# Performance work log

Hardware: AMD Instinct MI355X
Metric: run time of the kernel (lower is better)

## Reference

```python
import jax, jax.numpy as jnp
import numpy as np
from itertools import combinations

UNSPOOL = np.array([h + b for h in combinations(range(0, 4), 2) for b in combinations(range(4, 9), 3)])  # (60,5)
EMB = 64

def _lrelu(v):
    return jax.nn.leaky_relu(v, 0.01)

def _unspool(x):
    # x: (M,18) int -> (1,M,60,5) ranks, suits
    x = x[None]
    ranks, suits = x[:, :, ::2], x[:, :, 1::2]
    hr, hs = ranks[:, :, :4], suits[:, :, :4]
    br, bs = ranks[:, :, 4:], suits[:, :, 4:]
    hi, bi = jnp.argsort(hs, -1), jnp.argsort(bs, -1)
    hr = jnp.take_along_axis(hr, hi, -1); hs = jnp.take_along_axis(hs, hi, -1)
    br = jnp.take_along_axis(br, bi, -1); bs = jnp.take_along_axis(bs, bi, -1)
    hi2, bi2 = jnp.argsort(hr, -1), jnp.argsort(br, -1)
    r = jnp.concatenate([jnp.take_along_axis(hr, hi2, -1), jnp.take_along_axis(br, bi2, -1)], -1)
    s = jnp.concatenate([jnp.take_along_axis(hs, hi2, -1), jnp.take_along_axis(bs, bi2, -1)], -1)
    return r[:, :, UNSPOOL], s[:, :, UNSPOOL]

def setup_inputs() -> dict:
    key = jax.random.key(0)
    ks = jax.random.split(key, 24)
    M, nA = 2048, 9
    ranks = jax.random.randint(ks[0], (M, 9), 1, 14)
    suits = jax.random.randint(ks[1], (M, 9), 1, 5)
    x = jnp.zeros((M, 18), jnp.int64 if jax.config.jax_enable_x64 else jnp.int32)
    x = x.at[:, ::2].set(ranks).at[:, 1::2].set(suits)
    def lin(k, i, o):
        kw, kb = jax.random.split(k)
        s = 1.0 / np.sqrt(i)
        return (jax.random.uniform(kw, (i, o), jnp.float32, -s, s),
                jax.random.uniform(kb, (o,), jnp.float32, -s, s))
    emb = jax.random.normal(ks[2], (53, EMB), jnp.float32)
    emb = emb.at[0].set(0.0)  # padding_idx=0
    hW1, hb1 = lin(ks[3], 128, 512); hW2, hb2 = lin(ks[4], 512, 128)
    bW1, bb1 = lin(ks[5], 192, 512); bW2, bb2 = lin(ks[6], 512, 128)
    oW1, ob1 = lin(ks[7], 15360, 512); oW2, ob2 = lin(ks[8], 512, 256); oW3, ob3 = lin(ks[9], 256, 127)
    sW, sb = lin(ks[10], 127, nA)
    return dict(x=x, emb=emb, hW1=hW1, hb1=hb1, hW2=hW2, hb2=hb2,
                bW1=bW1, bb1=bb1, bW2=bW2, bb2=bb2,
                oW1=oW1, ob1=ob1, oW2=oW2, ob2=ob2, oW3=oW3, ob3=ob3,
                sW=sW, sb=sb)

def reference(x, emb, hW1, hb1, hW2, hb2, bW1, bb1, bW2, bb2,
              oW1, ob1, oW2, ob2, oW3, ob3, sW, sb):
    M = x.shape[0]
    sr, ss = _unspool(x)                      # (1,M,60,5)
    cards = (sr - 1) * ss                     # 0..48, 0 is padding
    e = emb[cards]                            # (1,M,60,5,64)
    hero = e[..., :2, :].reshape(1, M, 60, 2 * EMB)    # (1,M,60,128)
    board = e[..., 2:, :].reshape(1, M, 60, 3 * EMB)   # (1,M,60,192)
    hero = _lrelu(_lrelu(hero @ hW1 + hb1) @ hW2 + hb2)
    board = _lrelu(_lrelu(board @ bW1 + bb1) @ bW2 + bb2)
    raw = jnp.concatenate([hero, board], -1).reshape(1, M, 60 * 256)  # (1,M,15360)
    r = _lrelu(raw @ oW1 + ob1)
    r = _lrelu(r @ oW2 + ob2)
    r = _lrelu(r @ oW3 + ob3)
    return r.reshape(M, -1) @ sW + sb         # (M,nA)
```

## Files before the change

kernel.cpp:

```cpp
#include <hip/hip_runtime.h>

typedef _Float16 f16;
typedef __attribute__((ext_vector_type(8))) _Float16 f16x8;
typedef __attribute__((ext_vector_type(4))) _Float16 f16x4;
typedef __attribute__((ext_vector_type(4))) float f32x4;
typedef __attribute__((ext_vector_type(16))) float f32x16;

__device__ inline float lrelu(float v){ return v > 0.f ? v : 0.01f*v; }
__device__ inline f16x8 lrelu8(f16x8 v){
    f16x8 z = {};
    f16x8 mx = __builtin_elementwise_max(v, z);
    f16x8 mn = __builtin_elementwise_min(v, z);
    return mx + mn * (f16)0.01f;
}

__device__ __forceinline__ void gload16(const void* gp, void* lp) {
    __builtin_amdgcn_global_load_lds(
        (const __attribute__((address_space(1))) unsigned int*)gp,
        (__attribute__((address_space(3))) unsigned int*)lp,
        16, 0, 0);
}

#define M_ROWS 2048

#define P1_T    0
#define P1_HW2  265
#define P1_BW2  393
#define P1_OW2  521
#define P1_OW3  777
#define P1_CARD 841
#define P1_END  845

__device__ void d_transpose512(const float* __restrict__ in, f16* __restrict__ out,
                               int K, int Nin, int Nout, int b, int tid) {
    int idx = b * 512 + tid;
    if (idx >= Nout * K) return;
    int n = idx / K, k = idx - n * K;
    float v = (n < Nin) ? in[(size_t)k * Nin + n] : 0.f;
    out[idx] = (f16)v;
}

__global__ __launch_bounds__(512) void prep1(const int* __restrict__ x,
                                             const float* __restrict__ emb,
                                             const float* __restrict__ hW1,
                                             const float* __restrict__ hb1,
                                             const float* __restrict__ hW2,
                                             const float* __restrict__ bW1,
                                             const float* __restrict__ bb1,
                                             const float* __restrict__ bW2,
                                             const float* __restrict__ oW2,
                                             const float* __restrict__ oW3,
                                             f16* __restrict__ T,
                                             f16* __restrict__ hW2t,
                                             f16* __restrict__ bW2t,
                                             f16* __restrict__ oW2t,
                                             f16* __restrict__ oW3t,
                                             int* __restrict__ cid) {
    const int bid = blockIdx.x, tid = threadIdx.x;
    if (bid < P1_HW2) {
        int b = bid;
        int slot = b / 53, card = b - slot * 53;
        const float* W = (slot < 2) ? (hW1 + slot * 64 * 512) : (bW1 + (slot - 2) * 64 * 512);
        const float* e = emb + card * 64;
        float acc = (slot == 1) ? hb1[tid] : ((slot == 4) ? bb1[tid] : 0.f);
        #pragma unroll 8
        for (int k = 0; k < 64; ++k) acc += e[k] * W[k * 512 + tid];
        T[(size_t)b * 512 + tid] = (f16)acc;
    } else if (bid < P1_BW2) {
        d_transpose512(hW2, hW2t, 512, 128, 128, bid - P1_HW2, tid);
    } else if (bid < P1_OW2) {
        d_transpose512(bW2, bW2t, 512, 128, 128, bid - P1_BW2, tid);
    } else if (bid < P1_OW3) {
        d_transpose512(oW2, oW2t, 512, 256, 256, bid - P1_OW2, tid);
    } else if (bid < P1_CARD) {
        d_transpose512(oW3, oW3t, 256, 127, 128, bid - P1_OW3, tid);
    } else {
        int m = (bid - P1_CARD) * 512 + tid;
        if (m >= M_ROWS) return;
        int kh[4], kb[5];
        #pragma unroll
        for (int i = 0; i < 4; ++i) { int r = x[m*18 + 2*i], s = x[m*18 + 2*i + 1]; kh[i] = r*8 + s; }
        #pragma unroll
        for (int i = 0; i < 5; ++i) { int r = x[m*18 + 8 + 2*i], s = x[m*18 + 9 + 2*i]; kb[i] = r*8 + s; }
        #pragma unroll
        for (int i = 1; i < 4; ++i) { int v = kh[i], j = i-1; while (j >= 0 && kh[j] > v) { kh[j+1]=kh[j]; --j; } kh[j+1]=v; }
        #pragma unroll
        for (int i = 1; i < 5; ++i) { int v = kb[i], j = i-1; while (j >= 0 && kb[j] > v) { kb[j+1]=kb[j]; --j; } kb[j+1]=v; }
        #pragma unroll
        for (int i = 0; i < 4; ++i) { int r = kh[i] >> 3, s = kh[i] & 7; cid[m*9 + i] = (r - 1) * s; }
        #pragma unroll
        for (int i = 0; i < 5; ++i) { int r = kb[i] >> 3, s = kb[i] & 7; cid[m*9 + 4 + i] = (r - 1) * s; }
    }
}

#define MG_L2   256
#define MG_END  768

__global__ __launch_bounds__(512, 4) void mega(const int* __restrict__ cid,
                                               const f16* __restrict__ T,
                                               const f16* __restrict__ hW2t,
                                               const f16* __restrict__ bW2t,
                                               const float* __restrict__ hb2,
                                               const float* __restrict__ bb2,
                                               const float* __restrict__ oW1,
                                               f16* __restrict__ X,
                                               f16* __restrict__ Wct) {
    __shared__ __align__(16) char smem[51200];
    const int bid = blockIdx.x, tid = threadIdx.x;

    if (bid < MG_L2) {
        float (*tile)[65] = (float(*)[65])smem;
        int kb = bid & 31, nb = bid >> 5;
        int nl = tid & 63;
        for (int kl = tid >> 6; kl < 64; kl += 8) {
            int col = kb * 64 + kl;
            int p = col >> 7, r = col & 127;
            int n = nb * 64 + nl;
            float s = 0.f;
            if (p < 6) {
                #pragma unroll
                for (int j = 0; j < 10; ++j) s += oW1[(size_t)((p * 10 + j) * 256 + r) * 512 + n];
            } else {
                int t = p - 6;
                #pragma unroll
                for (int i = 0; i < 6; ++i) s += oW1[(size_t)((i * 10 + t) * 256 + 128 + r) * 512 + n];
            }
            tile[kl][nl] = s;
        }
        __syncthreads();
        for (int nl2 = tid >> 6; nl2 < 64; nl2 += 8) {
            int kl2 = tid & 63;
            Wct[(size_t)(nb * 64 + nl2) * 2048 + kb * 64 + kl2] = (f16)tile[kl2][nl2];
        }
        return;
    }

    f16 (*As)[64*64]  = (f16(*)[64*64])smem;
    f16 (*Bs)[128*64] = (f16(*)[128*64])(smem + 16384);
    const int lbid = bid - MG_L2;
    const bool hero = lbid < 192;
    const int row0 = hero ? lbid * 64 : (lbid - 192) * 64;
    const f16* Bt = hero ? hW2t : bW2t;
    const float* bias = hero ? hb2 : bb2;
    const int lane = tid & 63, wave = tid >> 6;
    const int rw = wave & 1, cw = wave >> 1;
    const int l31 = lane & 31, lh = lane >> 5;

    const int br = tid >> 3, bchunk = tid & 7;
    const int grow = row0 + br;
    const f16 *t0, *t1, *t2;
    if (hero) {
        const int HP0[6] = {0,0,0,1,1,2}, HP1[6] = {1,2,3,2,3,3};
        int m = grow / 6, p = grow - m * 6;
        t0 = T + (size_t)(0*53 + cid[m*9 + HP0[p]]) * 512;
        t1 = T + (size_t)(1*53 + cid[m*9 + HP1[p]]) * 512;
        t2 = T;
    } else {
        const int BT0[10] = {4,4,4,4,4,4,5,5,5,6};
        const int BT1[10] = {5,5,5,6,6,7,6,6,7,7};
        const int BT2[10] = {6,7,8,7,8,8,7,8,8,8};
        int m = grow / 10, t = grow - m * 10;
        t0 = T + (size_t)(2*53 + cid[m*9 + BT0[t]]) * 512;
        t1 = T + (size_t)(3*53 + cid[m*9 + BT1[t]]) * 512;
        t2 = T + (size_t)(4*53 + cid[m*9 + BT2[t]]) * 512;
    }

    auto stageB = [&](int buf, int k0) {
        #pragma unroll
        for (int i = 0; i < 2; ++i) {
            int c = tid + i * 512;
            int r = c >> 3, cc = c & 7;
            gload16(Bt + (size_t)r * 512 + k0 + ((cc ^ (r & 7)) << 3), (void*)&Bs[buf][c * 8]);
        }
    };
    auto buildA = [&](int buf, int k0) {
        f16x8 a = *(const f16x8*)(t0 + k0 + bchunk * 8);
        f16x8 b = *(const f16x8*)(t1 + k0 + bchunk * 8);
        f16x8 c = *(const f16x8*)(t2 + k0 + bchunk * 8);
        *(f16x8*)&As[buf][br * 64 + ((bchunk ^ (br & 7)) << 3)] = lrelu8(a + b + c);
    };

    f32x16 acc = {};
    stageB(0, 0); buildA(0, 0);
    __syncthreads();
    for (int t = 0; t < 8; ++t) {
        int cur = t & 1;
        if (t < 7) { stageB(cur ^ 1, (t + 1) * 64); buildA(cur ^ 1, (t + 1) * 64); }
        #pragma unroll
        for (int ks4 = 0; ks4 < 4; ++ks4) {
            int chunk = ks4 * 2 + lh;
            int ar = rw * 32 + l31, bcol = cw * 32 + l31;
            f16x8 a = *(const f16x8*)&As[cur][ar * 64 + ((chunk ^ (ar & 7)) << 3)];
            f16x8 b = *(const f16x8*)&Bs[cur][bcol * 64 + ((chunk ^ (bcol & 7)) << 3)];
            acc = __builtin_amdgcn_mfma_f32_32x32x16_f16(a, b, acc, 0, 0, 0);
        }
        __syncthreads();
    }
    #pragma unroll
    for (int q = 0; q < 16; ++q) {
        int row = row0 + rw * 32 + (q & 3) + 8 * (q >> 2) + 4 * lh;
        int col = cw * 32 + l31;
        float v = lrelu(acc[q] + bias[col]);
        size_t off;
        if (hero) { int m = row / 6,  p = row - m*6;  off = (size_t)m*2048 + p*128 + col; }
        else      { int m = row / 10, p = row - m*10; off = (size_t)m*2048 + 768 + p*128 + col; }
        X[off] = (f16)v;
    }
}

__global__ __launch_bounds__(512, 4) void combine(const f16* __restrict__ X,
                                                  const f16* __restrict__ Wct,
                                                  float* __restrict__ R1p) {
    __shared__ __align__(16) f16 As[2][64 * 64];
    __shared__ __align__(16) f16 Bs[2][128 * 64];
    const int bid = blockIdx.x;
    const int xcd = bid & 7, slot = bid >> 3;
    const int rp = xcd * 4 + (slot & 3);
    const int rest = slot >> 2;
    const int cp = rest & 3, ks = rest >> 2;
    const int row0 = rp * 64, col0 = cp * 128, k0b = ks * 512;
    const int tid = threadIdx.x, lane = tid & 63, wave = tid >> 6;
    const int rw = wave & 1, cw = wave >> 1;
    const int l31 = lane & 31, lh = lane >> 5;

    auto stage = [&](int buf, int k0) {
        { int r = tid >> 3, cc = tid & 7;
          gload16(X + (size_t)(row0 + r) * 2048 + k0 + ((cc ^ (r & 7)) << 3), (void*)&As[buf][tid * 8]); }
        #pragma unroll
        for (int i = 0; i < 2; ++i) {
            int c = tid + i * 512;
            int r = c >> 3, cc = c & 7;
            gload16(Wct + (size_t)(col0 + r) * 2048 + k0 + ((cc ^ (r & 7)) << 3), (void*)&Bs[buf][c * 8]);
        }
    };

    f32x16 acc = {};
    stage(0, k0b);
    __syncthreads();
    for (int t = 0; t < 8; ++t) {
        int cur = t & 1;
        if (t < 7) stage(cur ^ 1, k0b + (t + 1) * 64);
        #pragma unroll
        for (int ks4 = 0; ks4 < 4; ++ks4) {
            int chunk = ks4 * 2 + lh;
            int ar = rw * 32 + l31, bcol = cw * 32 + l31;
            f16x8 a = *(const f16x8*)&As[cur][ar * 64 + ((chunk ^ (ar & 7)) << 3)];
            f16x8 b = *(const f16x8*)&Bs[cur][bcol * 64 + ((chunk ^ (bcol & 7)) << 3)];
            acc = __builtin_amdgcn_mfma_f32_32x32x16_f16(a, b, acc, 0, 0, 0);
        }
        __syncthreads();
    }
    float* dst = R1p + (size_t)ks * 2048 * 512;
    #pragma unroll
    for (int q = 0; q < 16; ++q) {
        int row = row0 + rw * 32 + (q & 3) + 8 * (q >> 2) + 4 * lh;
        int col = col0 + cw * 32 + l31;
        dst[(size_t)row * 512 + col] = acc[q];
    }
}

__global__ __launch_bounds__(512, 2) void tail2(const float* __restrict__ R1p,
                                                const float* __restrict__ ob1,
                                                const f16* __restrict__ oW2t,
                                                const float* __restrict__ ob2,
                                                const f16* __restrict__ oW3t,
                                                const float* __restrict__ ob3,
                                                const float* __restrict__ sW,
                                                const float* __restrict__ sb,
                                                float* __restrict__ out) {
    __shared__ __align__(16) f16 A1s[16 * 512];
    __shared__ __align__(16) f16 Bs[2][256 * 64];
    __shared__ __align__(16) f16 R2s[16 * 256];
    __shared__ float R3s[16][132];
    __shared__ float sWs[127 * 9];
    __shared__ float sbs[9];
    const int row0 = blockIdx.x * 8;
    const int tid = threadIdx.x, lane = tid & 63, wave = tid >> 6;
    const int lr = lane & 15;

    auto stageB2 = [&](int buf, int t) {
        #pragma unroll
        for (int i = 0; i < 4; ++i) {
            int c = tid + i * 512;
            int r = c >> 3, cc = c & 7;
            gload16(oW2t + (size_t)r * 512 + t * 64 + ((cc ^ (r & 7)) << 3), (void*)&Bs[buf][c * 8]);
        }
    };
    stageB2(0, 0);

    #pragma unroll
    for (int i = 0; i < 2; ++i) {
        int g = tid + i * 512;
        int row = g >> 7, c4 = (g & 127) << 2;
        f32x4 v = *(const f32x4*)(ob1 + c4);
        #pragma unroll
        for (int s = 0; s < 4; ++s)
            v += *(const f32x4*)(R1p + (size_t)s * 2048 * 512 + (size_t)(row0 + row) * 512 + c4);
        f16x4 p;
        #pragma unroll
        for (int q = 0; q < 4; ++q) p[q] = (f16)lrelu(v[q]);
        int chunk = c4 >> 3, half = (c4 >> 2) & 1;
        *(f16x4*)&A1s[row * 512 + ((chunk ^ (row & 7)) << 3) + half * 4] = p;
    }
    {
        f16x8 z = {};
        int row = 8 + (tid >> 6), chunk = tid & 63;
        *(f16x8*)&A1s[row * 512 + chunk * 8] = z;
    }
    for (int i = tid; i < 127 * 9; i += 512) sWs[i] = sW[i];
    if (tid < 9) sbs[tid] = sb[tid];
    __syncthreads();

    f32x4 acc2[2] = {};
    for (int t = 0; t < 8; ++t) {
        int cur = t & 1;
        if (t < 7) stageB2(cur ^ 1, t + 1);
        #pragma unroll
        for (int kk2 = 0; kk2 < 2; ++kk2) {
            int g  = kk2 * 4 + (lane >> 4);
            int gg = t * 8 + g;
            f16x8 a = *(const f16x8*)&A1s[lr * 512 + ((gg ^ (lr & 7)) << 3)];
            int eo = (g ^ (lr & 7)) << 3;
            #pragma unroll
            for (int j = 0; j < 2; ++j) {
                f16x8 b = *(const f16x8*)&Bs[cur][(wave * 32 + j * 16 + lr) * 64 + eo];
                acc2[j] = __builtin_amdgcn_mfma_f32_16x16x32_f16(a, b, acc2[j], 0, 0, 0);
            }
        }
        __syncthreads();
    }
    #pragma unroll
    for (int j = 0; j < 2; ++j)
    #pragma unroll
    for (int q = 0; q < 4; ++q) {
        int row = (lane >> 4) * 4 + q;
        int col = wave * 32 + j * 16 + lr;
        f16 v = (f16)lrelu(acc2[j][q] + ob2[col]);
        int chunk = col >> 3, w = col & 7;
        R2s[row * 256 + ((chunk ^ (row & 7)) << 3) + w] = v;
    }
    auto stageB3 = [&](int buf, int t) {
        #pragma unroll
        for (int i = 0; i < 2; ++i) {
            int c = tid + i * 512;
            if (c < 1024) {
                int r = c >> 3, cc = c & 7;
                gload16(oW3t + (size_t)r * 256 + t * 64 + ((cc ^ (r & 7)) << 3), (void*)&Bs[buf][c * 8]);
            }
        }
    };
    stageB3(0, 0);
    __syncthreads();

    f32x4 acc3 = {};
    for (int t = 0; t < 4; ++t) {
        int cur = t & 1;
        if (t < 3) stageB3(cur ^ 1, t + 1);
        #pragma unroll
        for (int kk2 = 0; kk2 < 2; ++kk2) {
            int g  = kk2 * 4 + (lane >> 4);
            int gg = t * 8 + g;
            f16x8 a = *(const f16x8*)&R2s[lr * 256 + ((gg ^ (lr & 7)) << 3)];
            int eo = (g ^ (lr & 7)) << 3;
            f16x8 b = *(const f16x8*)&Bs[cur][(wave * 16 + lr) * 64 + eo];
            acc3 = __builtin_amdgcn_mfma_f32_16x16x32_f16(a, b, acc3, 0, 0, 0);
        }
        __syncthreads();
    }
    #pragma unroll
    for (int q = 0; q < 4; ++q) {
        int row = (lane >> 4) * 4 + q;
        int col = wave * 16 + lr;
        R3s[row][col] = lrelu(acc3[q] + ((col < 127) ? ob3[col] : 0.f));
    }
    __syncthreads();

    if (tid < 8 * 9) {
        int row = tid / 9, a = tid - row * 9;
        float s = sbs[a];
        #pragma unroll 4
        for (int n = 0; n < 127; ++n) s += R3s[row][n] * sWs[n * 9 + a];
        out[(size_t)(row0 + row) * 9 + a] = s;
    }
}

extern "C" void kernel_launch(void* const* d_in, const int* in_sizes, int n_in,
                              void* d_out, int out_size, void* d_ws, size_t ws_size,
                              hipStream_t stream) {
    const int*   x    = (const int*)  d_in[0];
    const float* emb  = (const float*)d_in[1];
    const float* hW1  = (const float*)d_in[2];
    const float* hb1  = (const float*)d_in[3];
    const float* hW2  = (const float*)d_in[4];
    const float* hb2  = (const float*)d_in[5];
    const float* bW1  = (const float*)d_in[6];
    const float* bb1  = (const float*)d_in[7];
    const float* bW2  = (const float*)d_in[8];
    const float* bb2  = (const float*)d_in[9];
    const float* oW1  = (const float*)d_in[10];
    const float* ob1  = (const float*)d_in[11];
    const float* oW2  = (const float*)d_in[12];
    const float* ob2  = (const float*)d_in[13];
    const float* oW3  = (const float*)d_in[14];
    const float* ob3  = (const float*)d_in[15];
    const float* sW   = (const float*)d_in[16];
    const float* sb   = (const float*)d_in[17];

    char* ws = (char*)d_ws;
    constexpr size_t OFF_T    = 0;
    constexpr size_t OFF_HW2T = 271360;
    constexpr size_t OFF_BW2T = 402432;
    constexpr size_t OFF_OW2T = 533504;
    constexpr size_t OFF_OW3T = 795648;
    constexpr size_t OFF_WCT  = 861184;
    constexpr size_t OFF_CID  = 2958336;
    constexpr size_t OFF_X    = 3032064;
    constexpr size_t OFF_R1P  = 11420672;

    f16*   T    = (f16*)(ws + OFF_T);
    f16*   hW2t = (f16*)(ws + OFF_HW2T);
    f16*   bW2t = (f16*)(ws + OFF_BW2T);
    f16*   oW2t = (f16*)(ws + OFF_OW2T);
    f16*   oW3t = (f16*)(ws + OFF_OW3T);
    f16*   Wct  = (f16*)(ws + OFF_WCT);
    int*   cid  = (int*)(ws + OFF_CID);
    f16*   X    = (f16*)(ws + OFF_X);
    float* R1p  = (float*)(ws + OFF_R1P);

    prep1<<<P1_END, 512, 0, stream>>>(x, emb, hW1, hb1, hW2, bW1, bb1, bW2,
                                      oW2, oW3, T, hW2t, bW2t, oW2t, oW3t, cid);
    mega<<<MG_END, 512, 0, stream>>>(cid, T, hW2t, bW2t, hb2, bb2, oW1, X, Wct);
    combine<<<512, 512, 0, stream>>>(X, Wct, R1p);
    tail2<<<256, 512, 0, stream>>>(R1p, ob1, oW2t, ob2, oW3t, ob3, sW, sb, (float*)d_out);
}
```

Before: 53.68 us.

## Move oW1 reduction into prep kernel and load tail weights directly from global

The oW1 column-sum reduction that builds Wct moves from the mega kernel into prep1, so mega only runs the hero/board MLP blocks. The tail2 kernel drops its LDS double-buffered staging of oW2t/oW3t and its per-step barriers. It reads weight fragments straight from global/L2, splits accumulators by parity to break MFMA dependency chains, and raises launch bounds occupancy to 4. The trade-off is uncoalesced direct global loads in tail2 and a heavier prep1 grid in place of shared-memory reuse.

```diff
diff --git a/kernel.cpp b/kernel.cpp
--- a/kernel.cpp
+++ b/kernel.cpp
@@ -23,13 +23,14 @@
 
 #define M_ROWS 2048
 
-#define P1_T    0
-#define P1_HW2  265
-#define P1_BW2  393
-#define P1_OW2  521
-#define P1_OW3  777
-#define P1_CARD 841
-#define P1_END  845
+#define P1_WCT  0
+#define P1_T    256
+#define P1_HW2  521
+#define P1_BW2  649
+#define P1_OW2  777
+#define P1_OW3  1033
+#define P1_CARD 1097
+#define P1_END  1101
 
 __device__ void d_transpose512(const float* __restrict__ in, f16* __restrict__ out,
                                int K, int Nin, int Nout, int b, int tid) {
@@ -48,6 +49,7 @@
                                              const float* __restrict__ bW1,
                                              const float* __restrict__ bb1,
                                              const float* __restrict__ bW2,
+                                             const float* __restrict__ oW1,
                                              const float* __restrict__ oW2,
                                              const float* __restrict__ oW3,
                                              f16* __restrict__ T,
@@ -55,10 +57,35 @@
                                              f16* __restrict__ bW2t,
                                              f16* __restrict__ oW2t,
                                              f16* __restrict__ oW3t,
+                                             f16* __restrict__ Wct,
                                              int* __restrict__ cid) {
+    __shared__ float tile[64][65];
     const int bid = blockIdx.x, tid = threadIdx.x;
-    if (bid < P1_HW2) {
-        int b = bid;
+    if (bid < P1_T) {
+        int kb = bid & 31, nb = bid >> 5;
+        int nl = tid & 63;
+        for (int kl = tid >> 6; kl < 64; kl += 8) {
+            int col = kb * 64 + kl;
+            int p = col >> 7, r = col & 127;
+            int n = nb * 64 + nl;
+            float s = 0.f;
+            if (p < 6) {
+                #pragma unroll
+                for (int j = 0; j < 10; ++j) s += oW1[(size_t)((p * 10 + j) * 256 + r) * 512 + n];
+            } else {
+                int t = p - 6;
+                #pragma unroll
+                for (int i = 0; i < 6; ++i) s += oW1[(size_t)((i * 10 + t) * 256 + 128 + r) * 512 + n];
+            }
+            tile[kl][nl] = s;
+        }
+        __syncthreads();
+        for (int nl2 = tid >> 6; nl2 < 64; nl2 += 8) {
+            int kl2 = tid & 63;
+            Wct[(size_t)(nb * 64 + nl2) * 2048 + kb * 64 + kl2] = (f16)tile[kl2][nl2];
+        }
+    } else if (bid < P1_HW2) {
+        int b = bid - P1_T;
         int slot = b / 53, card = b - slot * 53;
         const float* W = (slot < 2) ? (hW1 + slot * 64 * 512) : (bW1 + (slot - 2) * 64 * 512);
         const float* e = emb + card * 64;
@@ -93,53 +120,20 @@
     }
 }
 
-#define MG_L2   256
-#define MG_END  768
-
 __global__ __launch_bounds__(512, 4) void mega(const int* __restrict__ cid,
                                                const f16* __restrict__ T,
                                                const f16* __restrict__ hW2t,
                                                const f16* __restrict__ bW2t,
                                                const float* __restrict__ hb2,
                                                const float* __restrict__ bb2,
-                                               const float* __restrict__ oW1,
-                                               f16* __restrict__ X,
-                                               f16* __restrict__ Wct) {
+                                               f16* __restrict__ X) {
     __shared__ __align__(16) char smem[51200];
     const int bid = blockIdx.x, tid = threadIdx.x;
 
-    if (bid < MG_L2) {
-        float (*tile)[65] = (float(*)[65])smem;
-        int kb = bid & 31, nb = bid >> 5;
-        int nl = tid & 63;
-        for (int kl = tid >> 6; kl < 64; kl += 8) {
-            int col = kb * 64 + kl;
-            int p = col >> 7, r = col & 127;
-            int n = nb * 64 + nl;
-            float s = 0.f;
-            if (p < 6) {
-                #pragma unroll
-                for (int j = 0; j < 10; ++j) s += oW1[(size_t)((p * 10 + j) * 256 + r) * 512 + n];
-            } else {
-                int t = p - 6;
-                #pragma unroll
-                for (int i = 0; i < 6; ++i) s += oW1[(size_t)((i * 10 + t) * 256 + 128 + r) * 512 + n];
-            }
-            tile[kl][nl] = s;
-        }
-        __syncthreads();
-        for (int nl2 = tid >> 6; nl2 < 64; nl2 += 8) {
-            int kl2 = tid & 63;
-            Wct[(size_t)(nb * 64 + nl2) * 2048 + kb * 64 + kl2] = (f16)tile[kl2][nl2];
-        }
-        return;
-    }
-
     f16 (*As)[64*64]  = (f16(*)[64*64])smem;
     f16 (*Bs)[128*64] = (f16(*)[128*64])(smem + 16384);
-    const int lbid = bid - MG_L2;
-    const bool hero = lbid < 192;
-    const int row0 = hero ? lbid * 64 : (lbid - 192) * 64;
+    const bool hero = bid < 192;
+    const int row0 = hero ? bid * 64 : (bid - 192) * 64;
     const f16* Bt = hero ? hW2t : bW2t;
     const float* bias = hero ? hb2 : bb2;
     const int lane = tid & 63, wave = tid >> 6;
@@ -259,7 +253,7 @@
     }
 }
 
-__global__ __launch_bounds__(512, 2) void tail2(const float* __restrict__ R1p,
+__global__ __launch_bounds__(512, 4) void tail2(const float* __restrict__ R1p,
                                                 const float* __restrict__ ob1,
                                                 const f16* __restrict__ oW2t,
                                                 const float* __restrict__ ob2,
@@ -269,24 +263,13 @@
                                                 const float* __restrict__ sb,
                                                 float* __restrict__ out) {
     __shared__ __align__(16) f16 A1s[16 * 512];
-    __shared__ __align__(16) f16 Bs[2][256 * 64];
     __shared__ __align__(16) f16 R2s[16 * 256];
     __shared__ float R3s[16][132];
     __shared__ float sWs[127 * 9];
     __shared__ float sbs[9];
     const int row0 = blockIdx.x * 8;
     const int tid = threadIdx.x, lane = tid & 63, wave = tid >> 6;
-    const int lr = lane & 15;
-
-    auto stageB2 = [&](int buf, int t) {
-        #pragma unroll
-        for (int i = 0; i < 4; ++i) {
-            int c = tid + i * 512;
-            int r = c >> 3, cc = c & 7;
-            gload16(oW2t + (size_t)r * 512 + t * 64 + ((cc ^ (r & 7)) << 3), (void*)&Bs[buf][c * 8]);
-        }
-    };
-    stageB2(0, 0);
+    const int lr = lane & 15, lq = lane >> 4;
 
     #pragma unroll
     for (int i = 0; i < 2; ++i) {
@@ -311,67 +294,54 @@
     if (tid < 9) sbs[tid] = sb[tid];
     __syncthreads();
 
-    f32x4 acc2[2] = {};
+    const f16* pB0 = oW2t + (size_t)(wave * 32 + lr) * 512      + lq * 8;
+    const f16* pB1 = oW2t + (size_t)(wave * 32 + 16 + lr) * 512 + lq * 8;
+    f32x4 acc2[2][2] = {};
+    #pragma unroll
     for (int t = 0; t < 8; ++t) {
-        int cur = t & 1;
-        if (t < 7) stageB2(cur ^ 1, t + 1);
+        int par = t & 1;
         #pragma unroll
         for (int kk2 = 0; kk2 < 2; ++kk2) {
-            int g  = kk2 * 4 + (lane >> 4);
+            int g  = kk2 * 4 + lq;
             int gg = t * 8 + g;
-            f16x8 a = *(const f16x8*)&A1s[lr * 512 + ((gg ^ (lr & 7)) << 3)];
-            int eo = (g ^ (lr & 7)) << 3;
-            #pragma unroll
-            for (int j = 0; j < 2; ++j) {
-                f16x8 b = *(const f16x8*)&Bs[cur][(wave * 32 + j * 16 + lr) * 64 + eo];
-                acc2[j] = __builtin_amdgcn_mfma_f32_16x16x32_f16(a, b, acc2[j], 0, 0, 0);
-            }
-        }
-        __syncthreads();
+            f16x8 a  = *(const f16x8*)&A1s[lr * 512 + ((gg ^ (lr & 7)) << 3)];
+            f16x8 b0 = *(const f16x8*)(pB0 + t * 64 + kk2 * 32);
+            f16x8 b1 = *(const f16x8*)(pB1 + t * 64 + kk2 * 32);
+            acc2[0][par] = __builtin_amdgcn_mfma_f32_16x16x32_f16(a, b0, acc2[0][par], 0, 0, 0);
+            acc2[1][par] = __builtin_amdgcn_mfma_f32_16x16x32_f16(a, b1, acc2[1][par], 0, 0, 0);
+        }
     }
     #pragma unroll
     for (int j = 0; j < 2; ++j)
     #pragma unroll
     for (int q = 0; q < 4; ++q) {
-        int row = (lane >> 4) * 4 + q;
+        int row = lq * 4 + q;
         int col = wave * 32 + j * 16 + lr;
-        f16 v = (f16)lrelu(acc2[j][q] + ob2[col]);
+        f16 v = (f16)lrelu(acc2[j][0][q] + acc2[j][1][q] + ob2[col]);
         int chunk = col >> 3, w = col & 7;
         R2s[row * 256 + ((chunk ^ (row & 7)) << 3) + w] = v;
     }
-    auto stageB3 = [&](int buf, int t) {
-        #pragma unroll
-        for (int i = 0; i < 2; ++i) {
-            int c = tid + i * 512;
-            if (c < 1024) {
-                int r = c >> 3, cc = c & 7;
-                gload16(oW3t + (size_t)r * 256 + t * 64 + ((cc ^ (r & 7)) << 3), (void*)&Bs[buf][c * 8]);
-            }
-        }
-    };
-    stageB3(0, 0);
     __syncthreads();
 
-    f32x4 acc3 = {};
+    const f16* pC = oW3t + (size_t)(wave * 16 + lr) * 256 + lq * 8;
+    f32x4 acc3[2] = {};
+    #pragma unroll
     for (int t = 0; t < 4; ++t) {
-        int cur = t & 1;
-        if (t < 3) stageB3(cur ^ 1, t + 1);
+        int par = t & 1;
         #pragma unroll
         for (int kk2 = 0; kk2 < 2; ++kk2) {
-            int g  = kk2 * 4 + (lane >> 4);
+            int g  = kk2 * 4 + lq;
             int gg = t * 8 + g;
             f16x8 a = *(const f16x8*)&R2s[lr * 256 + ((gg ^ (lr & 7)) << 3)];
-            int eo = (g ^ (lr & 7)) << 3;
-            f16x8 b = *(const f16x8*)&Bs[cur][(wave * 16 + lr) * 64 + eo];
-            acc3 = __builtin_amdgcn_mfma_f32_16x16x32_f16(a, b, acc3, 0, 0, 0);
-        }
-        __syncthreads();
+            f16x8 b = *(const f16x8*)(pC + t * 64 + kk2 * 32);
+            acc3[par] = __builtin_amdgcn_mfma_f32_16x16x32_f16(a, b, acc3[par], 0, 0, 0);
+        }
     }
     #pragma unroll
     for (int q = 0; q < 4; ++q) {
-        int row = (lane >> 4) * 4 + q;
+        int row = lq * 4 + q;
         int col = wave * 16 + lr;
-        R3s[row][col] = lrelu(acc3[q] + ((col < 127) ? ob3[col] : 0.f));
+        R3s[row][col] = lrelu(acc3[0][q] + acc3[1][q] + ((col < 127) ? ob3[col] : 0.f));
     }
     __syncthreads();
 
@@ -428,8 +398,9 @@
     float* R1p  = (float*)(ws + OFF_R1P);
 
     prep1<<<P1_END, 512, 0, stream>>>(x, emb, hW1, hb1, hW2, bW1, bb1, bW2,
-                                      oW2, oW3, T, hW2t, bW2t, oW2t, oW3t, cid);
-    mega<<<MG_END, 512, 0, stream>>>(cid, T, hW2t, bW2t, hb2, bb2, oW1, X, Wct);
+                                      oW1, oW2, oW3,
+                                      T, hW2t, bW2t, oW2t, oW3t, Wct, cid);
+    mega<<<512, 512, 0, stream>>>(cid, T, hW2t, bW2t, hb2, bb2, X);
     combine<<<512, 512, 0, stream>>>(X, Wct, R1p);
     tail2<<<256, 512, 0, stream>>>(R1p, ob1, oW2t, ob2, oW3t, ob3, sW, sb, (float*)d_out);
 }
```

Result: slower. 56.51 us (+5.3%).
